# Kernel optimization log

Measured on AMD Instinct MI355X. Metric: run time of the kernel, lower is better.

Reference implementation:

```python
import jax, jax.numpy as jnp
import numpy as np

WS = 7        # window size
SHIFT = 3     # shift size
HEADS = 16
EPS = 1e-5


def _rel_pos_index(ws):
    coords = np.stack(np.meshgrid(np.arange(ws), np.arange(ws), indexing='ij')).reshape(2, -1)
    rel = (coords[:, :, None] - coords[:, None, :]).transpose(1, 2, 0).astype(np.int64)
    rel[..., 0] += ws - 1
    rel[..., 1] += ws - 1
    rel[..., 0] *= 2 * ws - 1
    return rel.sum(-1)  # (ws*ws, ws*ws)


def _attn_mask(H, W, ws, shift):
    if shift == 0:
        return None
    img = np.zeros((H, W), dtype=np.float32)
    cnt = 0
    slices = (slice(0, -ws), slice(-ws, -shift), slice(-shift, None))
    for hs in slices:
        for wsl in slices:
            img[hs, wsl] = cnt
            cnt += 1
    mw = img.reshape(H // ws, ws, W // ws, ws).transpose(0, 2, 1, 3).reshape(-1, ws * ws)
    diff = mw[:, None, :] - mw[:, :, None]  # matches unsqueeze(1) - unsqueeze(2)
    return jnp.asarray(np.where(diff != 0, -100.0, 0.0).astype(np.float32))  # (nW, N, N)


def _layernorm(x, g, b):
    mu = x.mean(-1, keepdims=True)
    var = ((x - mu) ** 2).mean(-1, keepdims=True)
    return (x - mu) * jax.lax.rsqrt(var + EPS) * g + b


def setup_inputs() -> dict:
    key = jax.random.key(0)
    ks = jax.random.split(key, 8)
    B, H, W, C = 32, 56, 56, 512
    hid = 4 * C
    s = 0.02
    return {
        'x': jax.random.normal(ks[0], (B, H * W, C), jnp.float32),
        'w_qkv': jax.random.normal(ks[1], (C, 3 * C), jnp.float32) * s,
        'b_qkv': jnp.zeros((3 * C,), jnp.float32),
        'w_proj': jax.random.normal(ks[2], (C, C), jnp.float32) * s,
        'b_proj': jnp.zeros((C,), jnp.float32),
        'bias_table': jax.random.normal(ks[3], ((2 * WS - 1) ** 2, HEADS), jnp.float32) * s,
        'ln1_g': jnp.ones((C,), jnp.float32),
        'ln1_b': jnp.zeros((C,), jnp.float32),
        'ln2_g': jnp.ones((C,), jnp.float32),
        'ln2_b': jnp.zeros((C,), jnp.float32),
        'w1': jax.random.normal(ks[4], (C, hid), jnp.float32) * s,
        'b1': jnp.zeros((hid,), jnp.float32),
        'w2': jax.random.normal(ks[5], (hid, C), jnp.float32) * s,
        'b2': jnp.zeros((C,), jnp.float32),
        'height': H,
        'width': W,
    }


def reference(x, w_qkv, b_qkv, w_proj, b_proj, bias_table, ln1_g, ln1_b, ln2_g, ln2_b,
              w1, b1, w2, b2, height, width):
    B, L, C = x.shape
    hd = C // HEADS
    N = WS * WS

    x2d = x.reshape(B, height, width, C)
    pad_b = (WS - height % WS) % WS
    pad_r = (WS - width % WS) % WS
    if pad_b or pad_r:
        x2d = jnp.pad(x2d, ((0, 0), (0, pad_b), (0, pad_r), (0, 0)))
    Hp, Wp = x2d.shape[1], x2d.shape[2]

    if SHIFT > 0:
        x2d = jnp.roll(x2d, (-SHIFT, -SHIFT), axis=(1, 2))

    nH, nW_ = Hp // WS, Wp // WS
    win = x2d.reshape(B, nH, WS, nW_, WS, C).transpose(0, 1, 3, 2, 4, 5).reshape(-1, N, C)
    BW = win.shape[0]

    h = _layernorm(win, ln1_g, ln1_b)
    qkv = (h @ w_qkv + b_qkv).reshape(BW, N, 3, HEADS, hd)
    q = qkv[:, :, 0].transpose(0, 2, 1, 3)  # (BW, heads, N, hd)
    k = qkv[:, :, 1].transpose(0, 2, 1, 3)
    v = qkv[:, :, 2].transpose(0, 2, 1, 3)

    scores = jnp.einsum('bhqd,bhkd->bhqk', q, k) * (hd ** -0.5)
    rpi = _rel_pos_index(WS)  # static numpy (N, N)
    rel_bias = bias_table[rpi.reshape(-1)].reshape(N, N, HEADS).transpose(2, 0, 1)
    scores = scores + rel_bias[None]

    mask = _attn_mask(Hp, Wp, WS, SHIFT)
    if mask is not None:
        nWin = mask.shape[0]
        scores = scores.reshape(BW // nWin, nWin, HEADS, N, N) + mask[None, :, None]
        scores = scores.reshape(BW, HEADS, N, N)

    attn = jax.nn.softmax(scores, axis=-1)
    out = jnp.einsum('bhqk,bhkd->bqhd', attn, v).reshape(BW, N, C)
    out = out @ w_proj + b_proj

    out = out.reshape(B, nH, nW_, WS, WS, C).transpose(0, 1, 3, 2, 4, 5).reshape(B, Hp, Wp, C)
    if SHIFT > 0:
        out = jnp.roll(out, (SHIFT, SHIFT), axis=(1, 2))
    if pad_b or pad_r:
        out = out[:, :height, :width]

    x = x + out.reshape(B, height * width, C)
    h2 = _layernorm(x, ln2_g, ln2_b)
    ff = jax.nn.gelu(h2 @ w1 + b1, approximate=False) @ w2 + b2
    return x + ff
```

## Files before the change

### kernel.cpp

```cpp
#include <hip/hip_runtime.h>
#include <hip/hip_bf16.h>
#include <cstdint>
#include <cstddef>


using s8v = __attribute__((ext_vector_type(8))) short;
using f4v = __attribute__((ext_vector_type(4))) float;

__device__ __forceinline__ short f2bf(float f) {
  union { __hip_bfloat16 h; short s; } u;
  u.h = __float2bfloat16(f);
  return u.s;
}

__device__ __forceinline__ f4v mfma16(s8v a, s8v b, f4v c) {
  return __builtin_amdgcn_mfma_f32_16x16x32_bf16(a, b, c, 0, 0, 0);
}

__device__ __forceinline__ f4v zero_f4() {
  f4v z; z[0] = 0.f; z[1] = 0.f; z[2] = 0.f; z[3] = 0.f; return z;
}
__device__ __forceinline__ s8v zero_s8() {
  s8v z;
#pragma unroll
  for (int i = 0; i < 8; ++i) z[i] = 0;
  return z;
}

__global__ __launch_bounds__(256) void transpose_w(const float* __restrict__ in,
                                                   short* __restrict__ outT,
                                                   int K, int N) {
  int idx = blockIdx.x * 256 + threadIdx.x;
  if (idx >= K * N) return;
  int k = idx / N, n = idx - k * N;
  outT[(size_t)n * K + k] = f2bf(in[idx]);
}

__global__ __launch_bounds__(256) void ln_kernel(const float* __restrict__ xin,
                                                 const float* __restrict__ g,
                                                 const float* __restrict__ bt,
                                                 short* __restrict__ outh,
                                                 int gather) {
  const int wid = threadIdx.x >> 6, lane = threadIdx.x & 63;
  const int m = blockIdx.x * 4 + wid;
  size_t src;
  if (gather) {
    int w = m / 49, n = m - w * 49;
    int b = w >> 6, wh = (w >> 3) & 7, ww = w & 7;
    int i = n / 7, j = n - i * 7;
    int r = wh * 7 + i + 3; if (r >= 56) r -= 56;
    int c = ww * 7 + j + 3; if (c >= 56) c -= 56;
    src = (size_t)b * 3136 + r * 56 + c;
  } else {
    src = m;
  }
  const float4* xp = (const float4*)(xin + src * 512) + lane * 2;
  float4 u0 = xp[0], u1 = xp[1];
  float vs[8] = {u0.x, u0.y, u0.z, u0.w, u1.x, u1.y, u1.z, u1.w};
  float s = 0.f;
#pragma unroll
  for (int e = 0; e < 8; ++e) s += vs[e];
#pragma unroll
  for (int msk = 1; msk < 64; msk <<= 1) s += __shfl_xor(s, msk, 64);
  const float mean = s * (1.0f / 512.0f);
  float ss = 0.f;
#pragma unroll
  for (int e = 0; e < 8; ++e) { float d = vs[e] - mean; ss += d * d; }
#pragma unroll
  for (int msk = 1; msk < 64; msk <<= 1) ss += __shfl_xor(ss, msk, 64);
  const float rstd = rsqrtf(ss * (1.0f / 512.0f) + 1e-5f);
  const float4* gp = (const float4*)g + lane * 2;
  const float4* bp = (const float4*)bt + lane * 2;
  float4 g0 = gp[0], g1 = gp[1], b0 = bp[0], b1 = bp[1];
  float gs[8] = {g0.x, g0.y, g0.z, g0.w, g1.x, g1.y, g1.z, g1.w};
  float bs[8] = {b0.x, b0.y, b0.z, b0.w, b1.x, b1.y, b1.z, b1.w};
  s8v o;
#pragma unroll
  for (int e = 0; e < 8; ++e) o[e] = f2bf((vs[e] - mean) * rstd * gs[e] + bs[e]);
  *(s8v*)(outh + (size_t)m * 512 + lane * 8) = o;
}

template <int EPI>
__global__ __launch_bounds__(256) void gemm_bt(const short* __restrict__ A,
                                               const short* __restrict__ BT,
                                               const float* __restrict__ bias,
                                               short* __restrict__ outb,
                                               const float* resid,
                                               float* outf,
                                               int K, int N) {
  __shared__ short As[128 * 64];
  __shared__ short Bs[128 * 64];
  const int tid = threadIdx.x;
  const int wid = tid >> 6, lane = tid & 63;
  const int lr = lane & 15, hi = lane >> 4;
  const int brow = blockIdx.y, bcol = blockIdx.x;
  const int r0 = (wid >> 1) * 64, c0 = (wid & 1) * 64;
  const int srow = lane >> 3, scol = (lane & 7) * 8;

  f4v acc[4][4];
#pragma unroll
  for (int a = 0; a < 4; ++a)
#pragma unroll
    for (int b = 0; b < 4; ++b) acc[a][b] = zero_f4();

  const short* Ab = A + (size_t)brow * 128 * K;
  const short* Bb = BT + (size_t)bcol * 128 * K;

  for (int k0 = 0; k0 < K; k0 += 64) {
#pragma unroll
    for (int i = 0; i < 4; ++i) {
      const int chunk = wid * 4 + i;
      const int row = chunk * 8 + srow;
      __builtin_amdgcn_global_load_lds(
          (const __attribute__((address_space(1))) void*)(Ab + (size_t)row * K + k0 + scol),
          (__attribute__((address_space(3))) void*)(As + chunk * 512), 16, 0, 0);
      __builtin_amdgcn_global_load_lds(
          (const __attribute__((address_space(1))) void*)(Bb + (size_t)row * K + k0 + scol),
          (__attribute__((address_space(3))) void*)(Bs + chunk * 512), 16, 0, 0);
    }
    __syncthreads();
#pragma unroll
    for (int kk = 0; kk < 64; kk += 32) {
      s8v af[4], bfr[4];
#pragma unroll
      for (int mi = 0; mi < 4; ++mi)
        af[mi] = *(const s8v*)(As + (r0 + mi * 16 + lr) * 64 + kk + hi * 8);
#pragma unroll
      for (int ni = 0; ni < 4; ++ni)
        bfr[ni] = *(const s8v*)(Bs + (c0 + ni * 16 + lr) * 64 + kk + hi * 8);
#pragma unroll
      for (int mi = 0; mi < 4; ++mi)
#pragma unroll
        for (int ni = 0; ni < 4; ++ni)
          acc[mi][ni] = mfma16(af[mi], bfr[ni], acc[mi][ni]);
    }
    __syncthreads();
  }

#pragma unroll
  for (int mi = 0; mi < 4; ++mi) {
#pragma unroll
    for (int ni = 0; ni < 4; ++ni) {
      const int col = bcol * 128 + c0 + ni * 16 + lr;
      const float bv = bias[col];
      f4v v = acc[mi][ni];
#pragma unroll
      for (int j = 0; j < 4; ++j) {
        const int row = brow * 128 + r0 + mi * 16 + hi * 4 + j;
        float val = v[j] + bv;
        if constexpr (EPI == 0) {
          outb[(size_t)row * N + col] = f2bf(val);
        } else if constexpr (EPI == 1) {
          int w = row / 49, n = row - w * 49;
          int b = w >> 6, wh = (w >> 3) & 7, ww = w & 7;
          int ii = n / 7, jj = n - ii * 7;
          int r = wh * 7 + ii + 3; if (r >= 56) r -= 56;
          int c = ww * 7 + jj + 3; if (c >= 56) c -= 56;
          size_t tok = (size_t)b * 3136 + r * 56 + c;
          outf[tok * 512 + col] = resid[tok * 512 + col] + val;
        } else if constexpr (EPI == 2) {
          float gv = 0.5f * val * (1.0f + erff(val * 0.70710678118654752f));
          outb[(size_t)row * N + col] = f2bf(gv);
        } else {
          outf[(size_t)row * 512 + col] = resid[(size_t)row * 512 + col] + val;
        }
      }
    }
  }
}

__device__ __forceinline__ int regof(int v) { return (v < 49) ? 0 : ((v < 53) ? 1 : 2); }

__global__ __launch_bounds__(64) void attn_kernel(const short* __restrict__ qkv,
                                                  const float* __restrict__ btab,
                                                  short* __restrict__ attno) {
  __shared__ short P[64 * 72];
  __shared__ short Vt[32 * 72];
  const int lane = threadIdx.x;
  const int w = blockIdx.x >> 4, head = blockIdx.x & 15;
  const int wh = (w >> 3) & 7, ww = w & 7;
  const int lr = lane & 15, hi = lane >> 4;

  s8v qf[4], kf[4];
#pragma unroll
  for (int t = 0; t < 4; ++t) {
    int row = t * 16 + lr;
    qf[t] = zero_s8();
    kf[t] = zero_s8();
    if (row < 49) {
      const short* base = qkv + (size_t)(w * 49 + row) * 1536 + head * 32 + hi * 8;
      qf[t] = *(const s8v*)base;
      kf[t] = *(const s8v*)(base + 512);
    }
  }

  f4v s[4][4];
  const f4v zacc = zero_f4();
#pragma unroll
  for (int qt = 0; qt < 4; ++qt)
#pragma unroll
    for (int kt = 0; kt < 4; ++kt) s[qt][kt] = mfma16(qf[qt], kf[kt], zacc);

  const float scale = 0.17677669529663687f;
  int ki_[4], kj_[4], labk_[4], kvalid[4];
#pragma unroll
  for (int kt = 0; kt < 4; ++kt) {
    int k = kt * 16 + lr;
    kvalid[kt] = (k < 49);
    int ki = k / 7, kj = k - ki * 7;
    ki_[kt] = ki; kj_[kt] = kj;
    labk_[kt] = regof(wh * 7 + ki) * 3 + regof(ww * 7 + kj);
  }
#pragma unroll
  for (int qt = 0; qt < 4; ++qt) {
#pragma unroll
    for (int j = 0; j < 4; ++j) {
      int q = qt * 16 + hi * 4 + j;
      int qvalid = (q < 49);
      int qi = q / 7, qj = q - qi * 7;
      int labq = regof(wh * 7 + qi) * 3 + regof(ww * 7 + qj);
#pragma unroll
      for (int kt = 0; kt < 4; ++kt) {
        float val = s[qt][kt][j] * scale;
        if (qvalid && kvalid[kt]) {
          int idx = (qi - ki_[kt] + 6) * 13 + (qj - kj_[kt] + 6);
          val += btab[idx * 16 + head];
          if (labq != labk_[kt]) val -= 100.f;
        }
        if (!kvalid[kt]) val = -1e30f;
        s[qt][kt][j] = val;
      }
    }
  }

#pragma unroll
  for (int qt = 0; qt < 4; ++qt) {
#pragma unroll
    for (int j = 0; j < 4; ++j) {
      float mx = fmaxf(fmaxf(s[qt][0][j], s[qt][1][j]), fmaxf(s[qt][2][j], s[qt][3][j]));
#pragma unroll
      for (int msk = 1; msk < 16; msk <<= 1) mx = fmaxf(mx, __shfl_xor(mx, msk, 64));
      float p[4], sum = 0.f;
#pragma unroll
      for (int kt = 0; kt < 4; ++kt) { p[kt] = __expf(s[qt][kt][j] - mx); sum += p[kt]; }
#pragma unroll
      for (int msk = 1; msk < 16; msk <<= 1) sum += __shfl_xor(sum, msk, 64);
      float inv = 1.f / sum;
      int q = qt * 16 + hi * 4 + j;
#pragma unroll
      for (int kt = 0; kt < 4; ++kt) P[q * 72 + kt * 16 + lr] = f2bf(p[kt] * inv);
    }
  }

  for (int idx = lane; idx < 2048; idx += 64) {
    int key = idx >> 5, d = idx & 31;
    short v = 0;
    if (key < 49) v = qkv[(size_t)(w * 49 + key) * 1536 + 1024 + head * 32 + d];
    Vt[d * 72 + key] = v;
  }
  __syncthreads();

  f4v o[4][2];
#pragma unroll
  for (int at = 0; at < 4; ++at)
#pragma unroll
    for (int dt = 0; dt < 2; ++dt) o[at][dt] = zero_f4();
#pragma unroll
  for (int ks = 0; ks < 2; ++ks) {
    s8v pa[4], vb[2];
#pragma unroll
    for (int at = 0; at < 4; ++at)
      pa[at] = *(const s8v*)(P + (at * 16 + lr) * 72 + ks * 32 + hi * 8);
#pragma unroll
    for (int dt = 0; dt < 2; ++dt)
      vb[dt] = *(const s8v*)(Vt + (dt * 16 + lr) * 72 + ks * 32 + hi * 8);
#pragma unroll
    for (int at = 0; at < 4; ++at)
#pragma unroll
      for (int dt = 0; dt < 2; ++dt) o[at][dt] = mfma16(pa[at], vb[dt], o[at][dt]);
  }

#pragma unroll
  for (int at = 0; at < 4; ++at)
#pragma unroll
    for (int dt = 0; dt < 2; ++dt)
#pragma unroll
      for (int j = 0; j < 4; ++j) {
        int q = at * 16 + hi * 4 + j;
        if (q < 49)
          attno[(size_t)(w * 49 + q) * 512 + head * 32 + dt * 16 + lr] = f2bf(o[at][dt][j]);
      }
}

extern "C" void kernel_launch(void* const* d_in, const int* in_sizes, int n_in,
                              void* d_out, int out_size, void* d_ws, size_t ws_size,
                              hipStream_t stream) {
  const float* x      = (const float*)d_in[0];
  const float* w_qkv  = (const float*)d_in[1];
  const float* b_qkv  = (const float*)d_in[2];
  const float* w_proj = (const float*)d_in[3];
  const float* b_proj = (const float*)d_in[4];
  const float* btab   = (const float*)d_in[5];
  const float* ln1g   = (const float*)d_in[6];
  const float* ln1b   = (const float*)d_in[7];
  const float* ln2g   = (const float*)d_in[8];
  const float* ln2b   = (const float*)d_in[9];
  const float* w1     = (const float*)d_in[10];
  const float* b1     = (const float*)d_in[11];
  const float* w2     = (const float*)d_in[12];
  const float* b2     = (const float*)d_in[13];
  float* out = (float*)d_out;

  char* ws = (char*)d_ws;
  short* wqkvT  = (short*)(ws + 0);
  short* wprojT = (short*)(ws + 1572864);
  short* w1T    = (short*)(ws + 2097152);
  short* w2T    = (short*)(ws + 4194304);
  short* bufH   = (short*)(ws + 6291456);
  short* qkvb   = (short*)(ws + 109051904);
  short* attno  = (short*)(ws + 417333248);
  short* hid    = qkvb;

  transpose_w<<<dim3(3072), 256, 0, stream>>>(w_qkv, wqkvT, 512, 1536);
  transpose_w<<<dim3(1024), 256, 0, stream>>>(w_proj, wprojT, 512, 512);
  transpose_w<<<dim3(4096), 256, 0, stream>>>(w1, w1T, 512, 2048);
  transpose_w<<<dim3(4096), 256, 0, stream>>>(w2, w2T, 2048, 512);

  ln_kernel<<<dim3(25088), 256, 0, stream>>>(x, ln1g, ln1b, bufH, 1);
  gemm_bt<0><<<dim3(12, 784), 256, 0, stream>>>(bufH, wqkvT, b_qkv, qkvb, nullptr, nullptr, 512, 1536);
  attn_kernel<<<dim3(32768), 64, 0, stream>>>(qkvb, btab, attno);
  gemm_bt<1><<<dim3(4, 784), 256, 0, stream>>>(attno, wprojT, b_proj, nullptr, x, out, 512, 512);
  ln_kernel<<<dim3(25088), 256, 0, stream>>>(out, ln2g, ln2b, bufH, 0);
  gemm_bt<2><<<dim3(16, 784), 256, 0, stream>>>(bufH, w1T, b1, hid, nullptr, nullptr, 512, 2048);
  gemm_bt<3><<<dim3(4, 784), 256, 0, stream>>>(hid, w2T, b2, nullptr, out, out, 2048, 512);
}
```

Before: 2.493 ms.

## Replace GEMM with 256x256 double-buffered 8-wave kernel with swizzled LDS

Replaces the 128x128 single-buffered GEMM with a 256x256 tile kernel using 8 waves, double-buffered LDS staging via global_load_lds, and an XOR-swizzled LDS layout to avoid bank conflicts. It also remaps block indices to group tiles for L2 locality and raises MFMA priority during compute. The aim is to overlap global loads with MFMA work and raise arithmetic intensity. In exchange it uses 128KB of LDS per block and more accumulator registers, which limits occupancy.

```diff
diff --git a/kernel.cpp b/kernel.cpp
--- a/kernel.cpp
+++ b/kernel.cpp
@@ -12,11 +12,9 @@
   u.h = __float2bfloat16(f);
   return u.s;
 }
-
 __device__ __forceinline__ f4v mfma16(s8v a, s8v b, f4v c) {
   return __builtin_amdgcn_mfma_f32_16x16x32_bf16(a, b, c, 0, 0, 0);
 }
-
 __device__ __forceinline__ f4v zero_f4() {
   f4v z; z[0] = 0.f; z[1] = 0.f; z[2] = 0.f; z[3] = 0.f; return z;
 }
@@ -81,72 +79,127 @@
 }
 
 template <int EPI>
-__global__ __launch_bounds__(256) void gemm_bt(const short* __restrict__ A,
-                                               const short* __restrict__ BT,
-                                               const float* __restrict__ bias,
-                                               short* __restrict__ outb,
-                                               const float* resid,
-                                               float* outf,
-                                               int K, int N) {
-  __shared__ short As[128 * 64];
-  __shared__ short Bs[128 * 64];
+__global__ __launch_bounds__(512, 2) void gemm8(const short* __restrict__ A,
+                                                const short* __restrict__ BT,
+                                                const float* __restrict__ bias,
+                                                short* __restrict__ outb,
+                                                const float* __restrict__ resid,
+                                                float* __restrict__ outf,
+                                                int K, int N, int NBC) {
+  __shared__ short As[2][2][128 * 64];
+  __shared__ short Bs[2][2][128 * 64];
   const int tid = threadIdx.x;
   const int wid = tid >> 6, lane = tid & 63;
   const int lr = lane & 15, hi = lane >> 4;
-  const int brow = blockIdx.y, bcol = blockIdx.x;
-  const int r0 = (wid >> 1) * 64, c0 = (wid & 1) * 64;
-  const int srow = lane >> 3, scol = (lane & 7) * 8;
-
-  f4v acc[4][4];
-#pragma unroll
-  for (int a = 0; a < 4; ++a)
+  const int wr = wid >> 2, wc = wid & 3;
+
+  const int cpx = gridDim.x >> 3;
+  const int flat = blockIdx.x;
+  const int swz = (flat & 7) * cpx + (flat >> 3);
+  const int bcol = swz % NBC, brow = swz / NBC;
+
+  const int srow_lo = wid * 8 + (lane >> 3);
+  const int scol_sw = ((lane & 7) ^ (lane >> 3)) * 8;
+
+  const short* Abase = A + (size_t)(brow * 256) * K;
+  const short* Bbase = BT + (size_t)(bcol * 256) * K;
+
+  auto stage_half = [&](int tensor, int h, int t, int buf) {
+    const short* gsrc = (tensor == 0 ? Abase : Bbase) +
+                        (size_t)(h * 128) * K + t * 64 + scol_sw;
+    short* ldst = (tensor == 0 ? &As[buf][h][0] : &Bs[buf][h][0]);
+#pragma unroll
+    for (int l = 0; l < 2; ++l) {
+      __builtin_amdgcn_global_load_lds(
+          (const __attribute__((address_space(1))) void*)(gsrc + (size_t)(l * 64 + srow_lo) * K),
+          (__attribute__((address_space(3))) void*)(ldst + l * 4096 + wid * 512), 16, 0, 0);
+    }
+  };
+
+  auto lda = [&](int buf, int mi, int ks) -> s8v {
+    const int row = mi * 16 + lr;
+    const int slot = (ks * 4 + hi) ^ (lr & 7);
+    return *(const s8v*)((const char*)&As[buf][wr][0] + row * 128 + slot * 16);
+  };
+  auto ldb = [&](int buf, int ni, int ks) -> s8v {
+    const int row = (wc & 1) * 64 + ni * 16 + lr;
+    const int slot = (ks * 4 + hi) ^ (lr & 7);
+    return *(const s8v*)((const char*)&Bs[buf][wc >> 1][0] + row * 128 + slot * 16);
+  };
+
+  f4v acc[8][4];
+#pragma unroll
+  for (int a = 0; a < 8; ++a)
 #pragma unroll
     for (int b = 0; b < 4; ++b) acc[a][b] = zero_f4();
 
-  const short* Ab = A + (size_t)brow * 128 * K;
-  const short* Bb = BT + (size_t)bcol * 128 * K;
-
-  for (int k0 = 0; k0 < K; k0 += 64) {
-#pragma unroll
-    for (int i = 0; i < 4; ++i) {
-      const int chunk = wid * 4 + i;
-      const int row = chunk * 8 + srow;
-      __builtin_amdgcn_global_load_lds(
-          (const __attribute__((address_space(1))) void*)(Ab + (size_t)row * K + k0 + scol),
-          (__attribute__((address_space(3))) void*)(As + chunk * 512), 16, 0, 0);
-      __builtin_amdgcn_global_load_lds(
-          (const __attribute__((address_space(1))) void*)(Bb + (size_t)row * K + k0 + scol),
-          (__attribute__((address_space(3))) void*)(Bs + chunk * 512), 16, 0, 0);
-    }
-    __syncthreads();
-#pragma unroll
-    for (int kk = 0; kk < 64; kk += 32) {
-      s8v af[4], bfr[4];
-#pragma unroll
-      for (int mi = 0; mi < 4; ++mi)
-        af[mi] = *(const s8v*)(As + (r0 + mi * 16 + lr) * 64 + kk + hi * 8);
-#pragma unroll
-      for (int ni = 0; ni < 4; ++ni)
-        bfr[ni] = *(const s8v*)(Bs + (c0 + ni * 16 + lr) * 64 + kk + hi * 8);
-#pragma unroll
-      for (int mi = 0; mi < 4; ++mi)
+#pragma unroll
+  for (int ht = 0; ht < 4; ++ht) stage_half(ht >> 1, ht & 1, 0, 0);
+
+  const int NT = K >> 6;
+  s8v bfrag[4];
+
+  for (int t = 0; t < NT - 1; ++t) {
+    const int buf = t & 1;
+#pragma unroll
+    for (int p = 0; p < 4; ++p) {
+      const int ks = p >> 1, mh = p & 1;
+      stage_half(p >> 1, p & 1, t + 1, buf ^ 1);
+      if (p == 0) asm volatile("s_waitcnt vmcnt(2)" ::: "memory");
+      __builtin_amdgcn_s_barrier();
+      if (mh == 0) {
+#pragma unroll
+        for (int ni = 0; ni < 4; ++ni) bfrag[ni] = ldb(buf, ni, ks);
+      }
+      s8v af[4];
+#pragma unroll
+      for (int m = 0; m < 4; ++m) af[m] = lda(buf, mh * 4 + m, ks);
+      __builtin_amdgcn_s_setprio(1);
+#pragma unroll
+      for (int m = 0; m < 4; ++m)
 #pragma unroll
         for (int ni = 0; ni < 4; ++ni)
-          acc[mi][ni] = mfma16(af[mi], bfr[ni], acc[mi][ni]);
-    }
-    __syncthreads();
-  }
-
-#pragma unroll
-  for (int mi = 0; mi < 4; ++mi) {
+          acc[mh * 4 + m][ni] = mfma16(af[m], bfrag[ni], acc[mh * 4 + m][ni]);
+      __builtin_amdgcn_s_setprio(0);
+      __builtin_amdgcn_s_barrier();
+    }
+  }
+
+  {
+    const int buf = (NT - 1) & 1;
+#pragma unroll
+    for (int p = 0; p < 4; ++p) {
+      const int ks = p >> 1, mh = p & 1;
+      if (p == 0) asm volatile("s_waitcnt vmcnt(0)" ::: "memory");
+      __builtin_amdgcn_s_barrier();
+      if (mh == 0) {
+#pragma unroll
+        for (int ni = 0; ni < 4; ++ni) bfrag[ni] = ldb(buf, ni, ks);
+      }
+      s8v af[4];
+#pragma unroll
+      for (int m = 0; m < 4; ++m) af[m] = lda(buf, mh * 4 + m, ks);
+      __builtin_amdgcn_s_setprio(1);
+#pragma unroll
+      for (int m = 0; m < 4; ++m)
+#pragma unroll
+        for (int ni = 0; ni < 4; ++ni)
+          acc[mh * 4 + m][ni] = mfma16(af[m], bfrag[ni], acc[mh * 4 + m][ni]);
+      __builtin_amdgcn_s_setprio(0);
+      __builtin_amdgcn_s_barrier();
+    }
+  }
+
+#pragma unroll
+  for (int mi = 0; mi < 8; ++mi) {
 #pragma unroll
     for (int ni = 0; ni < 4; ++ni) {
-      const int col = bcol * 128 + c0 + ni * 16 + lr;
+      const int col = bcol * 256 + wc * 64 + ni * 16 + lr;
       const float bv = bias[col];
       f4v v = acc[mi][ni];
 #pragma unroll
       for (int j = 0; j < 4; ++j) {
-        const int row = brow * 128 + r0 + mi * 16 + hi * 4 + j;
+        const int row = brow * 256 + wr * 128 + mi * 16 + hi * 4 + j;
         float val = v[j] + bv;
         if constexpr (EPI == 0) {
           outb[(size_t)row * N + col] = f2bf(val);
@@ -327,10 +380,10 @@
   transpose_w<<<dim3(4096), 256, 0, stream>>>(w2, w2T, 2048, 512);
 
   ln_kernel<<<dim3(25088), 256, 0, stream>>>(x, ln1g, ln1b, bufH, 1);
-  gemm_bt<0><<<dim3(12, 784), 256, 0, stream>>>(bufH, wqkvT, b_qkv, qkvb, nullptr, nullptr, 512, 1536);
+  gemm8<0><<<dim3(6 * 392), 512, 0, stream>>>(bufH, wqkvT, b_qkv, qkvb, nullptr, nullptr, 512, 1536, 6);
   attn_kernel<<<dim3(32768), 64, 0, stream>>>(qkvb, btab, attno);
-  gemm_bt<1><<<dim3(4, 784), 256, 0, stream>>>(attno, wprojT, b_proj, nullptr, x, out, 512, 512);
+  gemm8<1><<<dim3(2 * 392), 512, 0, stream>>>(attno, wprojT, b_proj, nullptr, x, out, 512, 512, 2);
   ln_kernel<<<dim3(25088), 256, 0, stream>>>(out, ln2g, ln2b, bufH, 0);
-  gemm_bt<2><<<dim3(16, 784), 256, 0, stream>>>(bufH, w1T, b1, hid, nullptr, nullptr, 512, 2048);
-  gemm_bt<3><<<dim3(4, 784), 256, 0, stream>>>(hid, w2T, b2, nullptr, out, out, 2048, 512);
-}
+  gemm8<2><<<dim3(8 * 392), 512, 0, stream>>>(bufH, w1T, b1, hid, nullptr, nullptr, 512, 2048, 8);
+  gemm8<3><<<dim3(2 * 392), 512, 0, stream>>>(hid, w2T, b2, nullptr, out, out, 2048, 512, 2);
+}
```

Result: faster. 2.426 ms (-2.7%).

## XOR-swizzle GEMM LDS tiles and remap blocks across XCDs

Applied to the files above, without the earlier changes.

The GEMM kernel now fills its LDS tiles with an XOR-swizzled column layout (chunk index XORed with the row within an 8-row group), and the fragment reads apply the same XOR. This is meant to remove LDS bank conflicts when 16 rows are read at the same 16-byte offset. Launches move to a 1D grid, and block ids are remapped so that consecutive tiles land on the same XCD, to improve L2 reuse of A and B tiles. resid and outf are also marked restrict. The remap assumes the grid size is divisible by 8, which holds for every launch here.

```diff
diff --git a/kernel.cpp b/kernel.cpp
--- a/kernel.cpp
+++ b/kernel.cpp
@@ -12,11 +12,9 @@
   u.h = __float2bfloat16(f);
   return u.s;
 }
-
 __device__ __forceinline__ f4v mfma16(s8v a, s8v b, f4v c) {
   return __builtin_amdgcn_mfma_f32_16x16x32_bf16(a, b, c, 0, 0, 0);
 }
-
 __device__ __forceinline__ f4v zero_f4() {
   f4v z; z[0] = 0.f; z[1] = 0.f; z[2] = 0.f; z[3] = 0.f; return z;
 }
@@ -85,26 +83,32 @@
                                                const short* __restrict__ BT,
                                                const float* __restrict__ bias,
                                                short* __restrict__ outb,
-                                               const float* resid,
-                                               float* outf,
-                                               int K, int N) {
+                                               const float* __restrict__ resid,
+                                               float* __restrict__ outf,
+                                               int K, int N, int NBC) {
   __shared__ short As[128 * 64];
   __shared__ short Bs[128 * 64];
   const int tid = threadIdx.x;
   const int wid = tid >> 6, lane = tid & 63;
   const int lr = lane & 15, hi = lane >> 4;
-  const int brow = blockIdx.y, bcol = blockIdx.x;
   const int r0 = (wid >> 1) * 64, c0 = (wid & 1) * 64;
-  const int srow = lane >> 3, scol = (lane & 7) * 8;
+
+  const int cpx = gridDim.x >> 3;
+  const int flat = blockIdx.x;
+  const int swz = (flat & 7) * cpx + (flat >> 3);
+  const int bcol = swz % NBC, brow = swz / NBC;
+
+  const int srow = lane >> 3;
+  const int scol_sw = ((lane & 7) ^ srow) * 8;
+
+  const short* Ab = A + (size_t)(brow * 128) * K;
+  const short* Bb = BT + (size_t)(bcol * 128) * K;
 
   f4v acc[4][4];
 #pragma unroll
   for (int a = 0; a < 4; ++a)
 #pragma unroll
     for (int b = 0; b < 4; ++b) acc[a][b] = zero_f4();
-
-  const short* Ab = A + (size_t)brow * 128 * K;
-  const short* Bb = BT + (size_t)bcol * 128 * K;
 
   for (int k0 = 0; k0 < K; k0 += 64) {
 #pragma unroll
@@ -112,22 +116,28 @@
       const int chunk = wid * 4 + i;
       const int row = chunk * 8 + srow;
       __builtin_amdgcn_global_load_lds(
-          (const __attribute__((address_space(1))) void*)(Ab + (size_t)row * K + k0 + scol),
+          (const __attribute__((address_space(1))) void*)(Ab + (size_t)row * K + k0 + scol_sw),
           (__attribute__((address_space(3))) void*)(As + chunk * 512), 16, 0, 0);
       __builtin_amdgcn_global_load_lds(
-          (const __attribute__((address_space(1))) void*)(Bb + (size_t)row * K + k0 + scol),
+          (const __attribute__((address_space(1))) void*)(Bb + (size_t)row * K + k0 + scol_sw),
           (__attribute__((address_space(3))) void*)(Bs + chunk * 512), 16, 0, 0);
     }
     __syncthreads();
 #pragma unroll
-    for (int kk = 0; kk < 64; kk += 32) {
+    for (int ks = 0; ks < 2; ++ks) {
       s8v af[4], bfr[4];
 #pragma unroll
-      for (int mi = 0; mi < 4; ++mi)
-        af[mi] = *(const s8v*)(As + (r0 + mi * 16 + lr) * 64 + kk + hi * 8);
-#pragma unroll
-      for (int ni = 0; ni < 4; ++ni)
-        bfr[ni] = *(const s8v*)(Bs + (c0 + ni * 16 + lr) * 64 + kk + hi * 8);
+      for (int mi = 0; mi < 4; ++mi) {
+        const int row = r0 + mi * 16 + lr;
+        const int slot = (ks * 4 + hi) ^ (lr & 7);
+        af[mi] = *(const s8v*)((const char*)As + row * 128 + slot * 16);
+      }
+#pragma unroll
+      for (int ni = 0; ni < 4; ++ni) {
+        const int row = c0 + ni * 16 + lr;
+        const int slot = (ks * 4 + hi) ^ (lr & 7);
+        bfr[ni] = *(const s8v*)((const char*)Bs + row * 128 + slot * 16);
+      }
 #pragma unroll
       for (int mi = 0; mi < 4; ++mi)
 #pragma unroll
@@ -327,10 +337,10 @@
   transpose_w<<<dim3(4096), 256, 0, stream>>>(w2, w2T, 2048, 512);
 
   ln_kernel<<<dim3(25088), 256, 0, stream>>>(x, ln1g, ln1b, bufH, 1);
-  gemm_bt<0><<<dim3(12, 784), 256, 0, stream>>>(bufH, wqkvT, b_qkv, qkvb, nullptr, nullptr, 512, 1536);
+  gemm_bt<0><<<dim3(12 * 784), 256, 0, stream>>>(bufH, wqkvT, b_qkv, qkvb, nullptr, nullptr, 512, 1536, 12);
   attn_kernel<<<dim3(32768), 64, 0, stream>>>(qkvb, btab, attno);
-  gemm_bt<1><<<dim3(4, 784), 256, 0, stream>>>(attno, wprojT, b_proj, nullptr, x, out, 512, 512);
+  gemm_bt<1><<<dim3(4 * 784), 256, 0, stream>>>(attno, wprojT, b_proj, nullptr, x, out, 512, 512, 4);
   ln_kernel<<<dim3(25088), 256, 0, stream>>>(out, ln2g, ln2b, bufH, 0);
-  gemm_bt<2><<<dim3(16, 784), 256, 0, stream>>>(bufH, w1T, b1, hid, nullptr, nullptr, 512, 2048);
-  gemm_bt<3><<<dim3(4, 784), 256, 0, stream>>>(hid, w2T, b2, nullptr, out, out, 2048, 512);
-}
+  gemm_bt<2><<<dim3(16 * 784), 256, 0, stream>>>(bufH, w1T, b1, hid, nullptr, nullptr, 512, 2048, 16);
+  gemm_bt<3><<<dim3(4 * 784), 256, 0, stream>>>(hid, w2T, b2, nullptr, out, out, 2048, 512, 4);
+}
```

Result: faster. 2.008 ms (-19.5%).
